# Optimization experiments

Hardware: AMD Instinct MI355X
Metric: run time of the kernel (lower is better)

## Reference

```python
import jax, jax.numpy as jnp
import numpy as np

N_NODES = 100000
N_EDGES = 1600000
IN_FEATS = 128
N_HIDDEN = 128
OUT_DIM = 32
BN_EPS = 1e-5


def setup_inputs() -> dict:
    key = jax.random.key(0)
    ks = jax.random.split(key, 12)
    s = 0.05  # weight init scale
    return {
        "features": jax.random.normal(ks[0], (N_NODES, IN_FEATS), dtype=jnp.float32),
        "src": jax.random.randint(ks[1], (N_EDGES,), 0, N_NODES),
        "dst": jax.random.randint(ks[2], (N_EDGES,), 0, N_NODES),
        # layer 0: in_feats -> n_hidden
        "Ws0": jax.random.normal(ks[3], (IN_FEATS, N_HIDDEN), dtype=jnp.float32) * s,
        "Wn0": jax.random.normal(ks[4], (IN_FEATS, N_HIDDEN), dtype=jnp.float32) * s,
        "b0": jnp.zeros((N_HIDDEN,), jnp.float32),
        # layer 1: n_hidden -> n_hidden
        "Ws1": jax.random.normal(ks[5], (N_HIDDEN, N_HIDDEN), dtype=jnp.float32) * s,
        "Wn1": jax.random.normal(ks[6], (N_HIDDEN, N_HIDDEN), dtype=jnp.float32) * s,
        "b1": jnp.zeros((N_HIDDEN,), jnp.float32),
        # layer 2 (output): n_hidden -> out_dim, no activation
        "Ws2": jax.random.normal(ks[7], (N_HIDDEN, OUT_DIM), dtype=jnp.float32) * s,
        "Wn2": jax.random.normal(ks[8], (N_HIDDEN, OUT_DIM), dtype=jnp.float32) * s,
        "b2": jnp.zeros((OUT_DIM,), jnp.float32),
        # batch norms after layers 0 and 1
        "g0": jnp.ones((N_HIDDEN,), jnp.float32),
        "be0": jnp.zeros((N_HIDDEN,), jnp.float32),
        "g1": jnp.ones((N_HIDDEN,), jnp.float32),
        "be1": jnp.zeros((N_HIDDEN,), jnp.float32),
    }


def _sage_mean(h, src, dst, inv_deg, Ws, Wn, b):
    # DGL SAGEConv('mean'): fc_self(h) + fc_neigh(mean of in-neighbor feats)
    agg = jax.ops.segment_sum(h[src], dst, num_segments=N_NODES) * inv_deg
    return h @ Ws + agg @ Wn + b


def _batch_norm(h, gamma, beta):
    mu = jnp.mean(h, axis=0)
    var = jnp.var(h, axis=0)
    return (h - mu) * jax.lax.rsqrt(var + BN_EPS) * gamma + beta


def reference(features, src, dst, Ws0, Wn0, b0, Ws1, Wn1, b1, Ws2, Wn2, b2, g0, be0, g1, be1):
    ones = jnp.ones((N_EDGES,), jnp.float32)
    deg = jax.ops.segment_sum(ones, dst, num_segments=N_NODES)
    inv_deg = (1.0 / jnp.maximum(deg, 1.0))[:, None]  # [N,1]

    # layer 0: SAGEConv internal activation, then BN + external activation
    h = jax.nn.relu(_sage_mean(features, src, dst, inv_deg, Ws0, Wn0, b0))
    h = jax.nn.relu(_batch_norm(h, g0, be0))
    # layer 1 (hidden)
    h = jax.nn.relu(_sage_mean(h, src, dst, inv_deg, Ws1, Wn1, b1))
    h = jax.nn.relu(_batch_norm(h, g1, be1))
    # layer 2 (output): no activation, no BN (idx > n_hidden_layers)
    h = _sage_mean(h, src, dst, inv_deg, Ws2, Wn2, b2)

    # dgl.mean_nodes over a single graph -> [1, out_dim], then softmax over classes
    hg = jnp.mean(h, axis=0, keepdims=True)
    return jax.nn.softmax(hg, axis=1)
```

## Files before the change

kernel.cpp:

```cpp
#include <hip/hip_runtime.h>
#include <hip/hip_bf16.h>

typedef __hip_bfloat16 bf16;
typedef __hip_bfloat162 bf162;

#define NN 100000
#define NE 1600000
#define BN_EPS 1e-5f

#define BSH 8
#define NBUCK ((NN + 255) >> BSH)
#define ABLK 128
#define EPBA ((NE + ABLK - 1) / ABLK)
#define CAP 6144

struct alignas(16) bf16x8 { bf16 v[8]; };

typedef __bf16 bfrag __attribute__((ext_vector_type(8)));
typedef float f4 __attribute__((ext_vector_type(4)));
typedef float f2 __attribute__((ext_vector_type(2)));

static __device__ __forceinline__ float b2f(bf16 x){ return __bfloat162float(x); }
static __device__ __forceinline__ bf16 f2b(float x){ return __float2bfloat16(x); }

static __device__ __forceinline__ uint2 pk8_fp8(float x0,float x1,float x2,float x3,
                                                float x4,float x5,float x6,float x7)
{
    int lo = __builtin_amdgcn_cvt_pk_fp8_f32(x0, x1, 0, 0);
    lo = __builtin_amdgcn_cvt_pk_fp8_f32(x2, x3, lo, 1);
    int hi = __builtin_amdgcn_cvt_pk_fp8_f32(x4, x5, 0, 0);
    hi = __builtin_amdgcn_cvt_pk_fp8_f32(x6, x7, hi, 1);
    return make_uint2((unsigned)lo, (unsigned)hi);
}

__global__ __launch_bounds__(256) void k_convert(const float* __restrict__ in, bf16* __restrict__ out,
                                                 unsigned char* __restrict__ outf8, int n)
{
    int i = (blockIdx.x * 256 + threadIdx.x) * 8;
    if (i + 7 < n) {
        float4 a = *(const float4*)(in + i);
        float4 b = *(const float4*)(in + i + 4);
        bf16x8 o;
        o.v[0]=f2b(a.x); o.v[1]=f2b(a.y); o.v[2]=f2b(a.z); o.v[3]=f2b(a.w);
        o.v[4]=f2b(b.x); o.v[5]=f2b(b.y); o.v[6]=f2b(b.z); o.v[7]=f2b(b.w);
        *(bf16x8*)(out + i) = o;
        *(uint2*)(outf8 + i) = pk8_fp8(a.x,a.y,a.z,a.w,b.x,b.y,b.z,b.w);
    }
}

__global__ __launch_bounds__(256) void k_wtrans(const float* __restrict__ W0, const float* __restrict__ W1,
                                                const float* __restrict__ W2, const float* __restrict__ W3,
                                                bf16* __restrict__ T0, bf16* __restrict__ T1,
                                                bf16* __restrict__ T2, bf16* __restrict__ T3)
{
    int m = blockIdx.x >> 6;
    int t = (blockIdx.x & 63) * 256 + threadIdx.x;
    const float* W = (m == 0) ? W0 : (m == 1) ? W1 : (m == 2) ? W2 : W3;
    bf16* T = (m == 0) ? T0 : (m == 1) ? T1 : (m == 2) ? T2 : T3;
    int n = t >> 7, k = t & 127;
    T[n * 128 + k] = f2b(W[k * 128 + n]);
}

__global__ __launch_bounds__(256) void k_pa1(const int* __restrict__ dst, const int* __restrict__ src,
                                             int* __restrict__ bucketCountD, int* __restrict__ blockBaseD,
                                             int* __restrict__ bucketCountS, int* __restrict__ blockBaseS)
{
    __shared__ int histD[NBUCK];
    __shared__ int histS[NBUCK];
    int t = threadIdx.x;
    for (int i = t; i < NBUCK; i += 256) { histD[i] = 0; histS[i] = 0; }
    __syncthreads();
    int e0 = blockIdx.x * EPBA, e1 = min(e0 + EPBA, NE);
    for (int e = e0 + t; e < e1; e += 256) {
        unsigned bd = ((unsigned)dst[e]) >> BSH;
        unsigned bs = ((unsigned)src[e]) >> BSH;
        if (bd < (unsigned)NBUCK) atomicAdd(&histD[bd], 1);
        if (bs < (unsigned)NBUCK) atomicAdd(&histS[bs], 1);
    }
    __syncthreads();
    for (int i = t; i < NBUCK; i += 256) {
        blockBaseD[blockIdx.x * NBUCK + i] = atomicAdd(&bucketCountD[i], histD[i]);
        blockBaseS[blockIdx.x * NBUCK + i] = atomicAdd(&bucketCountS[i], histS[i]);
    }
}

__global__ __launch_bounds__(512) void k_bscan2(const int* __restrict__ cntD, int* __restrict__ startD,
                                                const int* __restrict__ cntS, int* __restrict__ startS)
{
    __shared__ int sd[512];
    const int* cnt = (blockIdx.x == 0) ? cntD : cntS;
    int* start = (blockIdx.x == 0) ? startD : startS;
    int t = threadIdx.x;
    int v = (t < NBUCK) ? cnt[t] : 0;
    sd[t] = v;
    __syncthreads();
    for (int o = 1; o < 512; o <<= 1) {
        int x = (t >= o) ? sd[t - o] : 0;
        __syncthreads();
        sd[t] += x;
        __syncthreads();
    }
    if (t < NBUCK) start[t] = sd[t] - v;
    if (t == 0) start[NBUCK] = NE;
}

__global__ __launch_bounds__(256) void k_pa2(const int* __restrict__ src, const int* __restrict__ dst,
                                             const int* __restrict__ bucketStartD, const int* __restrict__ blockBaseD,
                                             const int* __restrict__ bucketStartS, const int* __restrict__ blockBaseS,
                                             uint2* __restrict__ pairsD, unsigned* __restrict__ packS)
{
    __shared__ int baseD[NBUCK];
    __shared__ int curD[NBUCK];
    __shared__ int baseS[NBUCK];
    __shared__ int curS[NBUCK];
    int t = threadIdx.x;
    for (int i = t; i < NBUCK; i += 256) {
        baseD[i] = bucketStartD[i] + blockBaseD[blockIdx.x * NBUCK + i];
        curD[i] = 0;
        baseS[i] = bucketStartS[i] + blockBaseS[blockIdx.x * NBUCK + i];
        curS[i] = 0;
    }
    __syncthreads();
    int e0 = blockIdx.x * EPBA, e1 = min(e0 + EPBA, NE);
    for (int e = e0 + t; e < e1; e += 256) {
        int s = src[e], d = dst[e];
        unsigned bd = ((unsigned)d) >> BSH;
        if (bd < (unsigned)NBUCK) {
            int r = atomicAdd(&curD[bd], 1);
            unsigned idx = (unsigned)(baseD[bd] + r);
            if (idx < (unsigned)NE) pairsD[idx] = make_uint2((unsigned)s, (unsigned)d);
        }
        unsigned bs = ((unsigned)s) >> BSH;
        if (bs < (unsigned)NBUCK) {
            int r = atomicAdd(&curS[bs], 1);
            unsigned idx = (unsigned)(baseS[bs] + r);
            if (idx < (unsigned)NE)
                packS[idx] = (((unsigned)s & 255u) << 24) | ((unsigned)d & 0xFFFFFFu);
        }
    }
}

__global__ __launch_bounds__(256) void k_pb1(const uint2* __restrict__ pairs, const int* __restrict__ bucketStart,
                                             int* __restrict__ offs, float* __restrict__ invd)
{
    __shared__ int dcnt[256];
    __shared__ int sscan[256];
    int t = threadIdx.x;
    dcnt[t] = 0;
    __syncthreads();
    int b = blockIdx.x;
    int base = b << BSH;
    int p0 = bucketStart[b], p1 = bucketStart[b + 1];
    for (int i = p0 + t; i < p1; i += 256) {
        unsigned li = pairs[i].y - (unsigned)base;
        if (li < 256u) atomicAdd(&dcnt[li], 1);
    }
    __syncthreads();
    int my = dcnt[t];
    sscan[t] = my;
    __syncthreads();
    for (int o = 1; o < 256; o <<= 1) {
        int v = (t >= o) ? sscan[t - o] : 0;
        __syncthreads();
        sscan[t] += v;
        __syncthreads();
    }
    if (base + t < NN) {
        offs[base + t] = p0 + (sscan[t] - my);
        invd[base + t] = 1.0f / (float)max(my, 1);
    }
    if (b == NBUCK - 1 && t == 0) offs[NN] = NE;
}

__global__ __launch_bounds__(256) void k_wsrc2(const unsigned* __restrict__ packS, const int* __restrict__ bucketStartS,
                                               const float* __restrict__ invd, float* __restrict__ wsrc)
{
    __shared__ float wacc[256];
    int t = threadIdx.x;
    wacc[t] = 0.f;
    __syncthreads();
    int b = blockIdx.x;
    int base = b << BSH;
    int p0 = bucketStartS[b], p1 = bucketStartS[b + 1];
    for (int i = p0 + t; i < p1; i += 256) {
        unsigned v = packS[i];
        unsigned li = v >> 24;
        unsigned dy = v & 0xFFFFFFu;
        if (dy >= (unsigned)NN) dy = 0u;
        atomicAdd(&wacc[li], invd[dy]);
    }
    __syncthreads();
    if (base + t < NN) wsrc[base + t] = wacc[t];
}

__global__ __launch_bounds__(256) void k_pb2(const uint2* __restrict__ pairs, const int* __restrict__ offs,
                                             int* __restrict__ esrc)
{
    __shared__ int loffs[257];
    __shared__ int cur[256];
    __shared__ int S[CAP];
    int t = threadIdx.x;
    int b = blockIdx.x;
    int base = b << BSH;
    int nEnd = min(base + 256, NN);
    int nn = nEnd - base;
    int o0 = offs[base];
    for (int i = t; i <= nn; i += 256) loffs[i] = offs[base + i] - o0;
    cur[t] = 0;
    for (int i = t; i < CAP; i += 256) S[i] = 0;
    __syncthreads();
    int cnt = loffs[nn];
    if (cnt <= CAP) {
        for (int i = t; i < cnt; i += 256) {
            uint2 pr = pairs[o0 + i];
            unsigned li = pr.y - (unsigned)base;
            if (li > 255u) li = 255u;
            int pos = loffs[li] + atomicAdd(&cur[li], 1);
            if ((unsigned)pos >= (unsigned)cnt) pos = cnt - 1;
            S[pos] = (int)pr.x;
        }
        __syncthreads();
        for (int i = t; i < cnt; i += 256) esrc[o0 + i] = S[i];
    } else {
        for (int i = t; i < cnt; i += 256) {
            uint2 pr = pairs[o0 + i];
            unsigned li = pr.y - (unsigned)base;
            if (li > 255u) li = 255u;
            int pos = loffs[li] + atomicAdd(&cur[li], 1);
            if ((unsigned)pos >= (unsigned)cnt) pos = cnt - 1;
            esrc[o0 + pos] = (int)pr.x;
        }
    }
}

__global__ __launch_bounds__(256) void k_aggregate(const unsigned char* __restrict__ inf8, bf16* __restrict__ out,
                                                   const int* __restrict__ offs, const int* __restrict__ esrc,
                                                   const float* __restrict__ invd,
                                                   const float* __restrict__ scsh, int use_ss)
{
    int row = blockIdx.x * 4 + (threadIdx.x >> 6);
    if (row >= NN) return;
    int lane = threadIdx.x & 63;
    int grp = lane >> 4;
    int c0 = (lane & 15) * 8;
    float sc[8], sh[8];
    if (use_ss) {
#pragma unroll
        for (int j = 0; j < 8; j++) { sc[j] = scsh[c0 + j]; sh[j] = scsh[128 + c0 + j]; }
    }
    int e0 = offs[row], e1 = offs[row + 1];
    float a[8];
#pragma unroll
    for (int j = 0; j < 8; j++) a[j] = 0.f;

    auto unpack = [&](uint2 u, float* v) {
        f2 p0 = __builtin_amdgcn_cvt_pk_f32_fp8(u.x, 0);
        f2 p1 = __builtin_amdgcn_cvt_pk_f32_fp8(u.x, 1);
        f2 p2 = __builtin_amdgcn_cvt_pk_f32_fp8(u.y, 0);
        f2 p3 = __builtin_amdgcn_cvt_pk_f32_fp8(u.y, 1);
        v[0]=p0.x; v[1]=p0.y; v[2]=p1.x; v[3]=p1.y; v[4]=p2.x; v[5]=p2.y; v[6]=p3.x; v[7]=p3.y;
    };

    int e = e0 + grp;
    for (; e + 12 < e1; e += 16) {
        int s0 = esrc[e], s1 = esrc[e + 4], s2 = esrc[e + 8], s3 = esrc[e + 12];
        uint2 u0 = *(const uint2*)&inf8[(size_t)s0 * 128 + c0];
        uint2 u1 = *(const uint2*)&inf8[(size_t)s1 * 128 + c0];
        uint2 u2 = *(const uint2*)&inf8[(size_t)s2 * 128 + c0];
        uint2 u3 = *(const uint2*)&inf8[(size_t)s3 * 128 + c0];
        float v0[8], v1[8], v2[8], v3[8];
        unpack(u0, v0); unpack(u1, v1); unpack(u2, v2); unpack(u3, v3);
        if (use_ss) {
#pragma unroll
            for (int j = 0; j < 8; j++)
                a[j] += fmaxf(v0[j] * sc[j] + sh[j], 0.f) + fmaxf(v1[j] * sc[j] + sh[j], 0.f)
                      + fmaxf(v2[j] * sc[j] + sh[j], 0.f) + fmaxf(v3[j] * sc[j] + sh[j], 0.f);
        } else {
#pragma unroll
            for (int j = 0; j < 8; j++)
                a[j] += (v0[j] + v1[j]) + (v2[j] + v3[j]);
        }
    }
    if (e < e1) {
        int i1 = e + 4, i2 = e + 8;
        float m1 = (i1 < e1) ? 1.f : 0.f;
        float m2 = (i2 < e1) ? 1.f : 0.f;
        if (i1 >= e1) i1 = e;
        if (i2 >= e1) i2 = e;
        int s0 = esrc[e], s1 = esrc[i1], s2 = esrc[i2];
        uint2 u0 = *(const uint2*)&inf8[(size_t)s0 * 128 + c0];
        uint2 u1 = *(const uint2*)&inf8[(size_t)s1 * 128 + c0];
        uint2 u2 = *(const uint2*)&inf8[(size_t)s2 * 128 + c0];
        float v0[8], v1[8], v2[8];
        unpack(u0, v0); unpack(u1, v1); unpack(u2, v2);
        if (use_ss) {
#pragma unroll
            for (int j = 0; j < 8; j++)
                a[j] += fmaxf(v0[j] * sc[j] + sh[j], 0.f)
                      + m1 * fmaxf(v1[j] * sc[j] + sh[j], 0.f)
                      + m2 * fmaxf(v2[j] * sc[j] + sh[j], 0.f);
        } else {
#pragma unroll
            for (int j = 0; j < 8; j++)
                a[j] += v0[j] + m1 * v1[j] + m2 * v2[j];
        }
    }
#pragma unroll
    for (int j = 0; j < 8; j++) {
        a[j] += __shfl_xor(a[j], 16);
        a[j] += __shfl_xor(a[j], 32);
    }
    if (grp == 0) {
        float id = invd[row];
        bf16x8 o;
#pragma unroll
        for (int j = 0; j < 8; j++) o.v[j] = f2b(a[j] * id);
        *(bf16x8*)&out[(size_t)row * 128 + c0] = o;
    }
}

#define GM 128
__global__ __launch_bounds__(256) void k_gemm_mfma(const bf16* __restrict__ Hs, const bf16* __restrict__ Ag,
                                                   const bf16* __restrict__ Wst, const bf16* __restrict__ Wnt,
                                                   const float* __restrict__ bias,
                                                   const float* __restrict__ scsh, int use_ss,
                                                   bf16* __restrict__ outp, unsigned char* __restrict__ outf8,
                                                   float* __restrict__ bnsums)
{
    __shared__ bf16 smem[2][128][72];
    __shared__ float sredsum[128], sredsq[128];
    int t = threadIdx.x;
    int row0 = blockIdx.x * GM;
    int lane = t & 63;
    int l16 = lane & 15;
    int quad = lane >> 4;
    int m0w = (t >> 6) * 32;

    if (t < 128) { sredsum[t] = 0.f; sredsq[t] = 0.f; }

    f4 acc[2][8];
#pragma unroll
    for (int rt = 0; rt < 2; rt++)
#pragma unroll
        for (int ct = 0; ct < 8; ct++) { f4 z = {0.f, 0.f, 0.f, 0.f}; acc[rt][ct] = z; }

    for (int kc = 0; kc < 128; kc += 64) {
#pragma unroll
        for (int i = 0; i < 4; i++) {
            int f = i * 256 + t;
            int row = f >> 3;
            int col8 = (f & 7) * 8;
            int grow = row0 + row;
            bf16x8 hv, av;
            if (grow < NN) {
                hv = *(const bf16x8*)&Hs[(size_t)grow * 128 + kc + col8];
                av = *(const bf16x8*)&Ag[(size_t)grow * 128 + kc + col8];
            } else {
#pragma unroll
                for (int j = 0; j < 8; j++) { hv.v[j] = f2b(0.f); av.v[j] = f2b(0.f); }
            }
            if (use_ss) {
#pragma unroll
                for (int j = 0; j < 8; j++) {
                    int k = kc + col8 + j;
                    hv.v[j] = f2b(fmaxf(b2f(hv.v[j]) * scsh[k] + scsh[128 + k], 0.f));
                }
            }
            *(bf16x8*)&smem[0][row][col8] = hv;
            *(bf16x8*)&smem[1][row][col8] = av;
        }
        __syncthreads();
#pragma unroll
        for (int ks2 = 0; ks2 < 2; ks2++) {
            int ko = ks2 * 32 + quad * 8;
            bfrag ah0 = *(const bfrag*)&smem[0][m0w + l16][ko];
            bfrag ah1 = *(const bfrag*)&smem[0][m0w + 16 + l16][ko];
            bfrag aa0 = *(const bfrag*)&smem[1][m0w + l16][ko];
            bfrag aa1 = *(const bfrag*)&smem[1][m0w + 16 + l16][ko];
            int kg = kc + ks2 * 32 + quad * 8;
#pragma unroll
            for (int ct = 0; ct < 8; ct++) {
                bfrag bs  = *(const bfrag*)&Wst[(ct * 16 + l16) * 128 + kg];
                bfrag bnf = *(const bfrag*)&Wnt[(ct * 16 + l16) * 128 + kg];
                acc[0][ct] = __builtin_amdgcn_mfma_f32_16x16x32_bf16(ah0, bs,  acc[0][ct], 0, 0, 0);
                acc[0][ct] = __builtin_amdgcn_mfma_f32_16x16x32_bf16(aa0, bnf, acc[0][ct], 0, 0, 0);
                acc[1][ct] = __builtin_amdgcn_mfma_f32_16x16x32_bf16(ah1, bs,  acc[1][ct], 0, 0, 0);
                acc[1][ct] = __builtin_amdgcn_mfma_f32_16x16x32_bf16(aa1, bnf, acc[1][ct], 0, 0, 0);
            }
        }
        __syncthreads();
    }

    bf16 (*sout)[136] = (bf16(*)[136])&smem[0][0][0];
    float psum[8], psq[8];
#pragma unroll
    for (int ct = 0; ct < 8; ct++) {
        float bv = bias[ct * 16 + l16];
        float s = 0.f, s2 = 0.f;
#pragma unroll
        for (int rt = 0; rt < 2; rt++) {
#pragma unroll
            for (int r = 0; r < 4; r++) {
                int lrow = m0w + rt * 16 + quad * 4 + r;
                float v = fmaxf(acc[rt][ct][r] + bv, 0.f);
                sout[lrow][ct * 16 + l16] = f2b(v);
                if (row0 + lrow < NN) { s += v; s2 += v * v; }
            }
        }
        psum[ct] = s; psq[ct] = s2;
    }
#pragma unroll
    for (int ct = 0; ct < 8; ct++) {
        psum[ct] += __shfl_xor(psum[ct], 16); psum[ct] += __shfl_xor(psum[ct], 32);
        psq[ct]  += __shfl_xor(psq[ct], 16);  psq[ct]  += __shfl_xor(psq[ct], 32);
    }
    if (lane < 16) {
#pragma unroll
        for (int ct = 0; ct < 8; ct++) {
            atomicAdd(&sredsum[ct * 16 + lane], psum[ct]);
            atomicAdd(&sredsq[ct * 16 + lane],  psq[ct]);
        }
    }
    __syncthreads();
#pragma unroll
    for (int i = 0; i < 8; i++) {
        int f = i * 256 + t;
        int row = f >> 4;
        int c16 = f & 15;
        int grow = row0 + row;
        if (grow < NN) {
            bf16x8 ov = *(const bf16x8*)&sout[row][c16 * 8];
            *(bf16x8*)&outp[(size_t)grow * 128 + c16 * 8] = ov;
            if (outf8) {
                *(uint2*)&outf8[(size_t)grow * 128 + c16 * 8] =
                    pk8_fp8(b2f(ov.v[0]), b2f(ov.v[1]), b2f(ov.v[2]), b2f(ov.v[3]),
                            b2f(ov.v[4]), b2f(ov.v[5]), b2f(ov.v[6]), b2f(ov.v[7]));
            }
        }
    }
    if (t < 128) {
        atomicAdd(&bnsums[t], sredsum[t]);
        atomicAdd(&bnsums[128 + t], sredsq[t]);
    }
}

__global__ void k_bn_fin(const float* __restrict__ sums, const float* __restrict__ g,
                         const float* __restrict__ be, float* __restrict__ scsh)
{
    int t = threadIdx.x;
    if (t < 128) {
        float mu = sums[t] / (float)NN;
        float var = sums[128 + t] / (float)NN - mu * mu;
        float sc = g[t] * rsqrtf(var + BN_EPS);
        scsh[t] = sc;
        scsh[128 + t] = be[t] - mu * sc;
    }
}

__global__ __launch_bounds__(256) void k_l2_reduce(const bf16* __restrict__ h, const float* __restrict__ scsh,
                                                   const float* __restrict__ wsrc, float* __restrict__ ue)
{
    __shared__ float su[128], se[128];
    int t = threadIdx.x;
    if (t < 128) { su[t] = 0.f; se[t] = 0.f; }
    __syncthreads();
    int c0 = (t & 15) * 8;
    int rof = t >> 4;
    float sc[8], sh[8];
#pragma unroll
    for (int j = 0; j < 8; j++) { sc[j] = scsh[c0 + j]; sh[j] = scsh[128 + c0 + j]; }
    float u[8], es[8];
#pragma unroll
    for (int j = 0; j < 8; j++) { u[j] = 0.f; es[j] = 0.f; }
    int rpb = (NN + gridDim.x - 1) / gridDim.x;
    int r0 = blockIdx.x * rpb;
    int r1 = min(r0 + rpb, NN);
    for (int r = r0 + rof; r < r1; r += 16) {
        bf16x8 v = *(const bf16x8*)&h[(size_t)r * 128 + c0];
        float w = wsrc[r];
#pragma unroll
        for (int j = 0; j < 8; j++) {
            float x = fmaxf(b2f(v.v[j]) * sc[j] + sh[j], 0.f);
            u[j] += x; es[j] += w * x;
        }
    }
#pragma unroll
    for (int j = 0; j < 8; j++) { atomicAdd(&su[c0 + j], u[j]); atomicAdd(&se[c0 + j], es[j]); }
    __syncthreads();
    if (t < 128) { atomicAdd(&ue[t], su[t]); atomicAdd(&ue[128 + t], se[t]); }
}

__global__ void k_final(const float* __restrict__ ue, const float* __restrict__ Ws2,
                        const float* __restrict__ Wn2, const float* __restrict__ b2,
                        float* __restrict__ out)
{
    __shared__ float logit[32];
    int t = threadIdx.x;
    const float inv = 1.0f / (float)NN;
    if (t < 32) {
        float acc = b2[t];
        for (int k = 0; k < 128; k++)
            acc += (ue[k] * inv) * Ws2[k * 32 + t] + (ue[128 + k] * inv) * Wn2[k * 32 + t];
        logit[t] = acc;
    }
    __syncthreads();
    if (t < 32) {
        float m = -1e30f;
        for (int j = 0; j < 32; j++) m = fmaxf(m, logit[j]);
        float s = 0.f;
        for (int j = 0; j < 32; j++) s += expf(logit[j] - m);
        out[t] = expf(logit[t] - m) / s;
    }
}

extern "C" void kernel_launch(void* const* d_in, const int* in_sizes, int n_in,
                              void* d_out, int out_size, void* d_ws, size_t ws_size,
                              hipStream_t stream)
{
    const float* feat = (const float*)d_in[0];
    const int*   src  = (const int*)d_in[1];
    const int*   dst  = (const int*)d_in[2];
    const float* Ws0  = (const float*)d_in[3];
    const float* Wn0  = (const float*)d_in[4];
    const float* b0   = (const float*)d_in[5];
    const float* Ws1  = (const float*)d_in[6];
    const float* Wn1  = (const float*)d_in[7];
    const float* b1   = (const float*)d_in[8];
    const float* Ws2  = (const float*)d_in[9];
    const float* Wn2  = (const float*)d_in[10];
    const float* b2   = (const float*)d_in[11];
    const float* g0   = (const float*)d_in[12];
    const float* be0  = (const float*)d_in[13];
    const float* g1   = (const float*)d_in[14];
    const float* be1  = (const float*)d_in[15];

    char* p = (char*)d_ws;
    auto alloc = [&](size_t b) -> void* {
        void* r = (void*)p;
        p += (b + 255) & ~(size_t)255;
        return r;
    };
    bf16* BB     = (bf16*)alloc((size_t)NN * 128 * 2);
    bf16* A      = (bf16*)alloc((size_t)NN * 128 * 2);
    unsigned char* F8 = (unsigned char*)alloc((size_t)NN * 128);
    unsigned* packS = (unsigned*)alloc((size_t)NE * 4);
    int*  offs   = (int*)alloc((size_t)(NN + 1) * 4);
    float* invd  = (float*)alloc((size_t)NN * 4);
    float* wsrc  = (float*)alloc((size_t)NN * 4);
    float* bn0   = (float*)alloc(256 * 4);
    float* scsh0 = (float*)alloc(256 * 4);
    float* bn1   = (float*)alloc(256 * 4);
    float* scsh1 = (float*)alloc(256 * 4);
    float* ue    = (float*)alloc(256 * 4);
    bf16* Ws0t   = (bf16*)alloc(16384 * 2);
    bf16* Wn0t   = (bf16*)alloc(16384 * 2);
    bf16* Ws1t   = (bf16*)alloc(16384 * 2);
    bf16* Wn1t   = (bf16*)alloc(16384 * 2);
    int*  bucketCountD = (int*)alloc((NBUCK + 1) * 4);
    int*  bucketStartD = (int*)alloc((NBUCK + 1) * 4);
    int*  blockBaseD   = (int*)alloc((size_t)ABLK * NBUCK * 4);
    int*  bucketCountS = (int*)alloc((NBUCK + 1) * 4);
    int*  bucketStartS = (int*)alloc((NBUCK + 1) * 4);
    int*  blockBaseS   = (int*)alloc((size_t)ABLK * NBUCK * 4);

    uint2* pairsD = (uint2*)A;
    int* esrc = (int*)packS;

    hipMemsetAsync(bucketCountD, 0, (NBUCK + 1) * 4, stream);
    hipMemsetAsync(bucketCountS, 0, (NBUCK + 1) * 4, stream);
    hipMemsetAsync(bn0, 0, 256 * 4, stream);
    hipMemsetAsync(bn1, 0, 256 * 4, stream);
    hipMemsetAsync(ue, 0, 256 * 4, stream);

    const int GB = (NN + GM - 1) / GM;

    k_convert<<<(NN * 128) / (256 * 8), 256, 0, stream>>>(feat, BB, F8, NN * 128);
    k_wtrans<<<256, 256, 0, stream>>>(Ws0, Wn0, Ws1, Wn1, Ws0t, Wn0t, Ws1t, Wn1t);

    k_pa1<<<ABLK, 256, 0, stream>>>(dst, src, bucketCountD, blockBaseD, bucketCountS, blockBaseS);
    k_bscan2<<<2, 512, 0, stream>>>(bucketCountD, bucketStartD, bucketCountS, bucketStartS);
    k_pa2<<<ABLK, 256, 0, stream>>>(src, dst, bucketStartD, blockBaseD, bucketStartS, blockBaseS, pairsD, packS);
    k_pb1<<<NBUCK, 256, 0, stream>>>(pairsD, bucketStartD, offs, invd);
    k_wsrc2<<<NBUCK, 256, 0, stream>>>(packS, bucketStartS, invd, wsrc);
    k_pb2<<<NBUCK, 256, 0, stream>>>(pairsD, offs, esrc);

    k_aggregate<<<(NN + 3) / 4, 256, 0, stream>>>(F8, A, offs, esrc, invd, nullptr, 0);
    k_gemm_mfma<<<GB, 256, 0, stream>>>(BB, A, Ws0t, Wn0t, b0, nullptr, 0, BB, F8, bn0);
    k_bn_fin<<<1, 128, 0, stream>>>(bn0, g0, be0, scsh0);

    k_aggregate<<<(NN + 3) / 4, 256, 0, stream>>>(F8, A, offs, esrc, invd, scsh0, 1);
    k_gemm_mfma<<<GB, 256, 0, stream>>>(BB, A, Ws1t, Wn1t, b1, scsh0, 1, A, nullptr, bn1);
    k_bn_fin<<<1, 128, 0, stream>>>(bn1, g1, be1, scsh1);

    k_l2_reduce<<<256, 256, 0, stream>>>(A, scsh1, wsrc, ue);
    k_final<<<1, 64, 0, stream>>>(ue, Ws2, Wn2, b2, (float*)d_out);
}
```

Baseline: 498.7 us.

## Pack dst edges to 32-bit, fuse CSR passes, drop bf16 feature copy

Destination-bucketed edges are now packed into 32-bit words (local dst in the high byte, src in the low 24 bits) instead of 8-byte pairs. The degree-count and CSR scatter kernels are merged into one, so the bucket is scanned in a single launch. The bf16 copy of the input features is removed: layer-0 GEMM reads fp32 features directly, and layer-1 GEMM reads the fp8 activations instead of the bf16 copy. The five small memsets become one. The aim is less memory traffic and fewer launches, at the cost of feeding layer 1 with lower-precision fp8 self features.

Result: faster. 481.3 us (-3.5%).

```diff
diff --git a/kernel.cpp b/kernel.cpp
--- a/kernel.cpp
+++ b/kernel.cpp
@@ -33,17 +33,13 @@
     return make_uint2((unsigned)lo, (unsigned)hi);
 }
 
-__global__ __launch_bounds__(256) void k_convert(const float* __restrict__ in, bf16* __restrict__ out,
+__global__ __launch_bounds__(256) void k_convert(const float* __restrict__ in,
                                                  unsigned char* __restrict__ outf8, int n)
 {
     int i = (blockIdx.x * 256 + threadIdx.x) * 8;
     if (i + 7 < n) {
         float4 a = *(const float4*)(in + i);
         float4 b = *(const float4*)(in + i + 4);
-        bf16x8 o;
-        o.v[0]=f2b(a.x); o.v[1]=f2b(a.y); o.v[2]=f2b(a.z); o.v[3]=f2b(a.w);
-        o.v[4]=f2b(b.x); o.v[5]=f2b(b.y); o.v[6]=f2b(b.z); o.v[7]=f2b(b.w);
-        *(bf16x8*)(out + i) = o;
         *(uint2*)(outf8 + i) = pk8_fp8(a.x,a.y,a.z,a.w,b.x,b.y,b.z,b.w);
     }
 }
@@ -107,7 +103,7 @@
 __global__ __launch_bounds__(256) void k_pa2(const int* __restrict__ src, const int* __restrict__ dst,
                                              const int* __restrict__ bucketStartD, const int* __restrict__ blockBaseD,
                                              const int* __restrict__ bucketStartS, const int* __restrict__ blockBaseS,
-                                             uint2* __restrict__ pairsD, unsigned* __restrict__ packS)
+                                             unsigned* __restrict__ packD, unsigned* __restrict__ packS)
 {
     __shared__ int baseD[NBUCK];
     __shared__ int curD[NBUCK];
@@ -128,7 +124,8 @@
         if (bd < (unsigned)NBUCK) {
             int r = atomicAdd(&curD[bd], 1);
             unsigned idx = (unsigned)(baseD[bd] + r);
-            if (idx < (unsigned)NE) pairsD[idx] = make_uint2((unsigned)s, (unsigned)d);
+            if (idx < (unsigned)NE)
+                packD[idx] = (((unsigned)d & 255u) << 24) | ((unsigned)s & 0xFFFFFFu);
         }
         unsigned bs = ((unsigned)s) >> BSH;
         if (bs < (unsigned)NBUCK) {
@@ -140,21 +137,25 @@
     }
 }
 
-__global__ __launch_bounds__(256) void k_pb1(const uint2* __restrict__ pairs, const int* __restrict__ bucketStart,
-                                             int* __restrict__ offs, float* __restrict__ invd)
+__global__ __launch_bounds__(256) void k_pbD(const unsigned* __restrict__ packD, const int* __restrict__ bucketStartD,
+                                             int* __restrict__ offs, float* __restrict__ invd,
+                                             int* __restrict__ esrc)
 {
     __shared__ int dcnt[256];
     __shared__ int sscan[256];
-    int t = threadIdx.x;
-    dcnt[t] = 0;
-    __syncthreads();
+    __shared__ int cur[256];
+    __shared__ int S[CAP];
+    int t = threadIdx.x;
     int b = blockIdx.x;
     int base = b << BSH;
-    int p0 = bucketStart[b], p1 = bucketStart[b + 1];
-    for (int i = p0 + t; i < p1; i += 256) {
-        unsigned li = pairs[i].y - (unsigned)base;
-        if (li < 256u) atomicAdd(&dcnt[li], 1);
-    }
+    dcnt[t] = 0;
+    cur[t] = 0;
+    for (int i = t; i < CAP; i += 256) S[i] = 0;
+    __syncthreads();
+    int p0 = bucketStartD[b], p1 = bucketStartD[b + 1];
+    int cnt = p1 - p0;
+    for (int i = p0 + t; i < p1; i += 256)
+        atomicAdd(&dcnt[packD[i] >> 24], 1);
     __syncthreads();
     int my = dcnt[t];
     sscan[t] = my;
@@ -165,11 +166,34 @@
         sscan[t] += v;
         __syncthreads();
     }
+    int lo = sscan[t] - my;
     if (base + t < NN) {
-        offs[base + t] = p0 + (sscan[t] - my);
+        offs[base + t] = p0 + lo;
         invd[base + t] = 1.0f / (float)max(my, 1);
     }
     if (b == NBUCK - 1 && t == 0) offs[NN] = NE;
+    __syncthreads();
+    sscan[t] = lo;
+    __syncthreads();
+    if (cnt <= CAP) {
+        for (int i = p0 + t; i < p1; i += 256) {
+            unsigned v = packD[i];
+            unsigned li = v >> 24;
+            int pos = sscan[li] + atomicAdd(&cur[li], 1);
+            if ((unsigned)pos >= (unsigned)cnt) pos = cnt - 1;
+            S[pos] = (int)(v & 0xFFFFFFu);
+        }
+        __syncthreads();
+        for (int i = t; i < cnt; i += 256) esrc[p0 + i] = S[i];
+    } else {
+        for (int i = p0 + t; i < p1; i += 256) {
+            unsigned v = packD[i];
+            unsigned li = v >> 24;
+            int pos = sscan[li] + atomicAdd(&cur[li], 1);
+            if ((unsigned)pos >= (unsigned)cnt) pos = cnt - 1;
+            esrc[p0 + pos] = (int)(v & 0xFFFFFFu);
+        }
+    }
 }
 
 __global__ __launch_bounds__(256) void k_wsrc2(const unsigned* __restrict__ packS, const int* __restrict__ bucketStartS,
@@ -191,46 +215,6 @@
     }
     __syncthreads();
     if (base + t < NN) wsrc[base + t] = wacc[t];
-}
-
-__global__ __launch_bounds__(256) void k_pb2(const uint2* __restrict__ pairs, const int* __restrict__ offs,
-                                             int* __restrict__ esrc)
-{
-    __shared__ int loffs[257];
-    __shared__ int cur[256];
-    __shared__ int S[CAP];
-    int t = threadIdx.x;
-    int b = blockIdx.x;
-    int base = b << BSH;
-    int nEnd = min(base + 256, NN);
-    int nn = nEnd - base;
-    int o0 = offs[base];
-    for (int i = t; i <= nn; i += 256) loffs[i] = offs[base + i] - o0;
-    cur[t] = 0;
-    for (int i = t; i < CAP; i += 256) S[i] = 0;
-    __syncthreads();
-    int cnt = loffs[nn];
-    if (cnt <= CAP) {
-        for (int i = t; i < cnt; i += 256) {
-            uint2 pr = pairs[o0 + i];
-            unsigned li = pr.y - (unsigned)base;
-            if (li > 255u) li = 255u;
-            int pos = loffs[li] + atomicAdd(&cur[li], 1);
-            if ((unsigned)pos >= (unsigned)cnt) pos = cnt - 1;
-            S[pos] = (int)pr.x;
-        }
-        __syncthreads();
-        for (int i = t; i < cnt; i += 256) esrc[o0 + i] = S[i];
-    } else {
-        for (int i = t; i < cnt; i += 256) {
-            uint2 pr = pairs[o0 + i];
-            unsigned li = pr.y - (unsigned)base;
-            if (li > 255u) li = 255u;
-            int pos = loffs[li] + atomicAdd(&cur[li], 1);
-            if ((unsigned)pos >= (unsigned)cnt) pos = cnt - 1;
-            esrc[o0 + pos] = (int)pr.x;
-        }
-    }
 }
 
 __global__ __launch_bounds__(256) void k_aggregate(const unsigned char* __restrict__ inf8, bf16* __restrict__ out,
@@ -320,7 +304,8 @@
 }
 
 #define GM 128
-__global__ __launch_bounds__(256) void k_gemm_mfma(const bf16* __restrict__ Hs, const bf16* __restrict__ Ag,
+__global__ __launch_bounds__(256) void k_gemm_mfma(const void* __restrict__ HsSrc, int hs_fp8,
+                                                   const bf16* __restrict__ Ag,
                                                    const bf16* __restrict__ Wst, const bf16* __restrict__ Wnt,
                                                    const float* __restrict__ bias,
                                                    const float* __restrict__ scsh, int use_ss,
@@ -351,21 +336,39 @@
             int row = f >> 3;
             int col8 = (f & 7) * 8;
             int grow = row0 + row;
-            bf16x8 hv, av;
+            float hv32[8];
+            bf16x8 av;
             if (grow < NN) {
-                hv = *(const bf16x8*)&Hs[(size_t)grow * 128 + kc + col8];
+                if (hs_fp8) {
+                    uint2 u = *(const uint2*)((const unsigned char*)HsSrc + (size_t)grow * 128 + kc + col8);
+                    f2 q0 = __builtin_amdgcn_cvt_pk_f32_fp8(u.x, 0);
+                    f2 q1 = __builtin_amdgcn_cvt_pk_f32_fp8(u.x, 1);
+                    f2 q2 = __builtin_amdgcn_cvt_pk_f32_fp8(u.y, 0);
+                    f2 q3 = __builtin_amdgcn_cvt_pk_f32_fp8(u.y, 1);
+                    hv32[0]=q0.x; hv32[1]=q0.y; hv32[2]=q1.x; hv32[3]=q1.y;
+                    hv32[4]=q2.x; hv32[5]=q2.y; hv32[6]=q3.x; hv32[7]=q3.y;
+                } else {
+                    const float* fp = (const float*)HsSrc + (size_t)grow * 128 + kc + col8;
+                    float4 x = *(const float4*)fp;
+                    float4 y = *(const float4*)(fp + 4);
+                    hv32[0]=x.x; hv32[1]=x.y; hv32[2]=x.z; hv32[3]=x.w;
+                    hv32[4]=y.x; hv32[5]=y.y; hv32[6]=y.z; hv32[7]=y.w;
+                }
                 av = *(const bf16x8*)&Ag[(size_t)grow * 128 + kc + col8];
             } else {
 #pragma unroll
-                for (int j = 0; j < 8; j++) { hv.v[j] = f2b(0.f); av.v[j] = f2b(0.f); }
+                for (int j = 0; j < 8; j++) { hv32[j] = 0.f; av.v[j] = f2b(0.f); }
             }
             if (use_ss) {
 #pragma unroll
                 for (int j = 0; j < 8; j++) {
                     int k = kc + col8 + j;
-                    hv.v[j] = f2b(fmaxf(b2f(hv.v[j]) * scsh[k] + scsh[128 + k], 0.f));
+                    hv32[j] = fmaxf(hv32[j] * scsh[k] + scsh[128 + k], 0.f);
                 }
             }
+            bf16x8 hv;
+#pragma unroll
+            for (int j = 0; j < 8; j++) hv.v[j] = f2b(hv32[j]);
             *(bf16x8*)&smem[0][row][col8] = hv;
             *(bf16x8*)&smem[1][row][col8] = av;
         }
@@ -430,7 +433,7 @@
         int grow = row0 + row;
         if (grow < NN) {
             bf16x8 ov = *(const bf16x8*)&sout[row][c16 * 8];
-            *(bf16x8*)&outp[(size_t)grow * 128 + c16 * 8] = ov;
+            if (outp) *(bf16x8*)&outp[(size_t)grow * 128 + c16 * 8] = ov;
             if (outf8) {
                 *(uint2*)&outf8[(size_t)grow * 128 + c16 * 8] =
                     pk8_fp8(b2f(ov.v[0]), b2f(ov.v[1]), b2f(ov.v[2]), b2f(ov.v[3]),
@@ -540,56 +543,52 @@
         p += (b + 255) & ~(size_t)255;
         return r;
     };
-    bf16* BB     = (bf16*)alloc((size_t)NN * 128 * 2);
     bf16* A      = (bf16*)alloc((size_t)NN * 128 * 2);
     unsigned char* F8 = (unsigned char*)alloc((size_t)NN * 128);
     unsigned* packS = (unsigned*)alloc((size_t)NE * 4);
+    int*  esrc   = (int*)alloc((size_t)NE * 4);
     int*  offs   = (int*)alloc((size_t)(NN + 1) * 4);
     float* invd  = (float*)alloc((size_t)NN * 4);
     float* wsrc  = (float*)alloc((size_t)NN * 4);
+    char* zstart = p;
+    int*  bucketCountD = (int*)alloc((NBUCK + 1) * 4);
+    int*  bucketCountS = (int*)alloc((NBUCK + 1) * 4);
     float* bn0   = (float*)alloc(256 * 4);
+    float* bn1   = (float*)alloc(256 * 4);
+    float* ue    = (float*)alloc(256 * 4);
+    size_t zlen = (size_t)(p - zstart);
     float* scsh0 = (float*)alloc(256 * 4);
-    float* bn1   = (float*)alloc(256 * 4);
     float* scsh1 = (float*)alloc(256 * 4);
-    float* ue    = (float*)alloc(256 * 4);
     bf16* Ws0t   = (bf16*)alloc(16384 * 2);
     bf16* Wn0t   = (bf16*)alloc(16384 * 2);
     bf16* Ws1t   = (bf16*)alloc(16384 * 2);
     bf16* Wn1t   = (bf16*)alloc(16384 * 2);
-    int*  bucketCountD = (int*)alloc((NBUCK + 1) * 4);
     int*  bucketStartD = (int*)alloc((NBUCK + 1) * 4);
+    int*  bucketStartS = (int*)alloc((NBUCK + 1) * 4);
     int*  blockBaseD   = (int*)alloc((size_t)ABLK * NBUCK * 4);
-    int*  bucketCountS = (int*)alloc((NBUCK + 1) * 4);
-    int*  bucketStartS = (int*)alloc((NBUCK + 1) * 4);
     int*  blockBaseS   = (int*)alloc((size_t)ABLK * NBUCK * 4);
 
-    uint2* pairsD = (uint2*)A;
-    int* esrc = (int*)packS;
-
-    hipMemsetAsync(bucketCountD, 0, (NBUCK + 1) * 4, stream);
-    hipMemsetAsync(bucketCountS, 0, (NBUCK + 1) * 4, stream);
-    hipMemsetAsync(bn0, 0, 256 * 4, stream);
-    hipMemsetAsync(bn1, 0, 256 * 4, stream);
-    hipMemsetAsync(ue, 0, 256 * 4, stream);
+    unsigned* packD = (unsigned*)A;
+
+    hipMemsetAsync(zstart, 0, zlen, stream);
 
     const int GB = (NN + GM - 1) / GM;
 
-    k_convert<<<(NN * 128) / (256 * 8), 256, 0, stream>>>(feat, BB, F8, NN * 128);
+    k_convert<<<(NN * 128) / (256 * 8), 256, 0, stream>>>(feat, F8, NN * 128);
     k_wtrans<<<256, 256, 0, stream>>>(Ws0, Wn0, Ws1, Wn1, Ws0t, Wn0t, Ws1t, Wn1t);
 
     k_pa1<<<ABLK, 256, 0, stream>>>(dst, src, bucketCountD, blockBaseD, bucketCountS, blockBaseS);
     k_bscan2<<<2, 512, 0, stream>>>(bucketCountD, bucketStartD, bucketCountS, bucketStartS);
-    k_pa2<<<ABLK, 256, 0, stream>>>(src, dst, bucketStartD, blockBaseD, bucketStartS, blockBaseS, pairsD, packS);
-    k_pb1<<<NBUCK, 256, 0, stream>>>(pairsD, bucketStartD, offs, invd);
+    k_pa2<<<ABLK, 256, 0, stream>>>(src, dst, bucketStartD, blockBaseD, bucketStartS, blockBaseS, packD, packS);
+    k_pbD<<<NBUCK, 256, 0, stream>>>(packD, bucketStartD, offs, invd, esrc);
     k_wsrc2<<<NBUCK, 256, 0, stream>>>(packS, bucketStartS, invd, wsrc);
-    k_pb2<<<NBUCK, 256, 0, stream>>>(pairsD, offs, esrc);
 
     k_aggregate<<<(NN + 3) / 4, 256, 0, stream>>>(F8, A, offs, esrc, invd, nullptr, 0);
-    k_gemm_mfma<<<GB, 256, 0, stream>>>(BB, A, Ws0t, Wn0t, b0, nullptr, 0, BB, F8, bn0);
+    k_gemm_mfma<<<GB, 256, 0, stream>>>(feat, 0, A, Ws0t, Wn0t, b0, nullptr, 0, nullptr, F8, bn0);
     k_bn_fin<<<1, 128, 0, stream>>>(bn0, g0, be0, scsh0);
 
     k_aggregate<<<(NN + 3) / 4, 256, 0, stream>>>(F8, A, offs, esrc, invd, scsh0, 1);
-    k_gemm_mfma<<<GB, 256, 0, stream>>>(BB, A, Ws1t, Wn1t, b1, scsh0, 1, A, nullptr, bn1);
+    k_gemm_mfma<<<GB, 256, 0, stream>>>(F8, 1, A, Ws1t, Wn1t, b1, scsh0, 1, A, nullptr, bn1);
     k_bn_fin<<<1, 128, 0, stream>>>(bn1, g1, be1, scsh1);
 
     k_l2_reduce<<<256, 256, 0, stream>>>(A, scsh1, wsrc, ue);
```
